# Kernel tuning notes

Hardware: AMD Instinct MI355X
Metric: run time of the kernel (lower is better)

Reference implementation:

```python
import jax, jax.numpy as jnp
import numpy as np

NX, NY, NT = 128, 128, 64          # global space-time grid
LX, LY = 2.0, 2.0                  # periodic domain extents
K_NB = 128                         # neighbors per query
NHEAD = 4
EPS = 1e-5


def setup_inputs() -> dict:
    key = jax.random.key(0)
    ks = jax.random.split(key, 12)
    N = NX * NY * NT
    B, d, dff, L = 2048, 64, 128, 2
    nrm = lambda k, s: jax.random.normal(k, s, jnp.float32) * 0.05
    return {
        "q_lin_idx": jax.random.randint(ks[0], (B,), 0, N),
        "offsets_ijk": jax.random.randint(ks[1], (K_NB, 3), 0, 8),
        "coords": jax.random.uniform(ks[2], (N, 3), jnp.float32) * 2.0,
        "vals": jax.random.normal(ks[3], (N, 3), jnp.float32),
        "log_gammas": jnp.zeros((3,), jnp.float32),
        "proj_w": nrm(ks[4], (d, 6)), "proj_b": jnp.zeros((d,), jnp.float32),
        "qkv_w": nrm(ks[5], (L, 3 * d, d)), "qkv_b": jnp.zeros((L, 3 * d), jnp.float32),
        "out_w": nrm(ks[6], (L, d, d)), "out_b": jnp.zeros((L, d), jnp.float32),
        "ln1_s": jnp.ones((L, d), jnp.float32), "ln1_b": jnp.zeros((L, d), jnp.float32),
        "ff1_w": nrm(ks[7], (L, dff, d)), "ff1_b": jnp.zeros((L, dff), jnp.float32),
        "ff2_w": nrm(ks[8], (L, d, dff)), "ff2_b": jnp.zeros((L, d), jnp.float32),
        "ln2_s": jnp.ones((L, d), jnp.float32), "ln2_b": jnp.zeros((L, d), jnp.float32),
        "head_ln_s": jnp.ones((d,), jnp.float32), "head_ln_b": jnp.zeros((d,), jnp.float32),
        "head1_w": nrm(ks[9], (d, d)), "head1_b": jnp.zeros((d,), jnp.float32),
        "head2_w": nrm(ks[10], (3, d)), "head2_b": jnp.zeros((3,), jnp.float32),
    }


def _ln(x, s, b):
    m = x.mean(-1, keepdims=True)
    v = ((x - m) ** 2).mean(-1, keepdims=True)
    return (x - m) * jax.lax.rsqrt(v + EPS) * s + b


def _dper(a, b, L):
    # periodic relative delta in [-L/2, L/2)
    return (a - b + 0.5 * L) % L - 0.5 * L


def reference(q_lin_idx, offsets_ijk, coords, vals, log_gammas, proj_w, proj_b,
              qkv_w, qkv_b, out_w, out_b, ln1_s, ln1_b, ff1_w, ff1_b, ff2_w, ff2_b,
              ln2_s, ln2_b, head_ln_s, head_ln_b, head1_w, head1_b, head2_w, head2_b):
    # --- periodic-wrapped neighbor indices (div/mod on linear index) ---
    i = q_lin_idx // (NY * NT)
    r = q_lin_idx % (NY * NT)
    j = r // NT
    kk = r % NT
    di, dj, dk = offsets_ijk[:, 0], offsets_ijk[:, 1], offsets_ijk[:, 2]
    I = (i[:, None] + di[None, :]) % NX          # wrap_x
    J = (j[:, None] + dj[None, :]) % NY          # wrap_y
    T = jnp.clip(kk[:, None] + dk[None, :], 0, NT - 1)  # no wrap in t
    nb = I * (NY * NT) + J * NT + T              # [B, K]

    # --- gather + relative-delta encode ---
    q_xyz = coords[q_lin_idx]                    # [B, 3]
    nb_xyz = coords[nb]                          # [B, K, 3]
    dx = _dper(nb_xyz[..., 0], q_xyz[:, None, 0], LX)
    dy = _dper(nb_xyz[..., 1], q_xyz[:, None, 1], LY)
    dt = nb_xyz[..., 2] - q_xyz[:, None, 2]
    rel = jnp.stack([dx, dy, dt], -1) * jnp.exp(log_gammas)[None, None, :]
    tokens = jnp.concatenate([rel, vals[nb]], -1)  # [B, K, 6]

    # --- input projection + TransformerEncoder (post-norm, relu FF) ---
    h = tokens @ proj_w.T + proj_b               # [B, S, d]
    B, S, d = h.shape
    dh = d // NHEAD
    scale = 1.0 / np.sqrt(dh).astype(np.float32)
    for l in range(qkv_w.shape[0]):
        qkv = h @ qkv_w[l].T + qkv_b[l]
        qh, kh, vh = jnp.split(qkv, 3, axis=-1)
        qh = qh.reshape(B, S, NHEAD, dh).transpose(0, 2, 1, 3)
        kh = kh.reshape(B, S, NHEAD, dh).transpose(0, 2, 1, 3)
        vh = vh.reshape(B, S, NHEAD, dh).transpose(0, 2, 1, 3)
        att = jax.nn.softmax(jnp.einsum('bhqd,bhkd->bhqk', qh, kh) * scale, axis=-1)
        o = jnp.einsum('bhqk,bhkd->bhqd', att, vh).transpose(0, 2, 1, 3).reshape(B, S, d)
        h = _ln(h + (o @ out_w[l].T + out_b[l]), ln1_s[l], ln1_b[l])
        ff = jax.nn.relu(h @ ff1_w[l].T + ff1_b[l]) @ ff2_w[l].T + ff2_b[l]
        h = _ln(h + ff, ln2_s[l], ln2_b[l])

    # --- mean pool over neighbors + head ---
    hm = h.mean(axis=1)                          # [B, d]
    g = _ln(hm, head_ln_s, head_ln_b)
    g = jax.nn.gelu(g @ head1_w.T + head1_b, approximate=False)
    return g @ head2_w.T + head2_b               # [B, 3]
```

## Files before the change

### kernel.cpp

```cpp
#include <hip/hip_runtime.h>
#include <math.h>

#define NXg 128
#define NYg 128
#define NTg 64
#define SEQ 128
#define DIM 64
#define NH 4
#define DHd 16
#define DFFd 128
#define NLAYER 2
#define EPSf 1e-5f

typedef _Float16 f16x8 __attribute__((ext_vector_type(8)));
typedef _Float16 f16x4 __attribute__((ext_vector_type(4)));
typedef float f32x4 __attribute__((ext_vector_type(4)));

#define MFMA16(a, b, c) __builtin_amdgcn_mfma_f32_16x16x32_f16(a, b, c, 0, 0, 0)

__device__ __forceinline__ f16x8 zero8() {
  f16x8 z;
#pragma unroll
  for (int i = 0; i < 8; ++i) z[i] = (_Float16)0.0f;
  return z;
}
__device__ __forceinline__ f16x8 ld8(const _Float16* p) { return *(const f16x8*)p; }

__global__ void prep_weights(const float* __restrict__ qkv_w,
                             const float* __restrict__ out_w,
                             const float* __restrict__ ff1_w,
                             const float* __restrict__ ff2_w,
                             _Float16* __restrict__ wsH) {
  int i = blockIdx.x * 256 + threadIdx.x;
  if (i < 24576) wsH[i] = (_Float16)qkv_w[i];
  else if (i < 32768) wsH[i] = (_Float16)out_w[i - 24576];
  else if (i < 49152) wsH[i] = (_Float16)ff1_w[i - 32768];
  else if (i < 65536) wsH[i] = (_Float16)ff2_w[i - 49152];
}

__device__ __forceinline__ void res_ln_T(f32x4 acc[4][2],
                                         const float* __restrict__ bias,
                                         const float* __restrict__ lns,
                                         const float* __restrict__ lnb,
                                         _Float16* sX,
                                         int wv, int quad, int l15) {
  f32x4 bb[4], sv[4], bv[4];
#pragma unroll
  for (int mt = 0; mt < 4; ++mt) {
    bb[mt] = *(const f32x4*)(bias + mt * 16 + quad * 4);
    sv[mt] = *(const f32x4*)(lns + mt * 16 + quad * 4);
    bv[mt] = *(const f32x4*)(lnb + mt * 16 + quad * 4);
  }
#pragma unroll
  for (int qt = 0; qt < 2; ++qt) {
    const int q = (wv * 2 + qt) * 16 + l15;
    float v[4][4];
#pragma unroll
    for (int mt = 0; mt < 4; ++mt) {
      f16x4 rx = *(const f16x4*)(sX + q * 72 + mt * 16 + quad * 4);
#pragma unroll
      for (int jr = 0; jr < 4; ++jr)
        v[mt][jr] = acc[mt][qt][jr] + bb[mt][jr] + (float)rx[jr];
    }
    float s = 0.f;
#pragma unroll
    for (int mt = 0; mt < 4; ++mt)
#pragma unroll
      for (int jr = 0; jr < 4; ++jr) s += v[mt][jr];
    s += __shfl_xor(s, 16, 64);
    s += __shfl_xor(s, 32, 64);
    const float mu = s * (1.0f / 64.0f);
    float q2 = 0.f;
#pragma unroll
    for (int mt = 0; mt < 4; ++mt)
#pragma unroll
      for (int jr = 0; jr < 4; ++jr) { float d = v[mt][jr] - mu; q2 = fmaf(d, d, q2); }
    q2 += __shfl_xor(q2, 16, 64);
    q2 += __shfl_xor(q2, 32, 64);
    const float rstd = rsqrtf(q2 * (1.0f / 64.0f) + EPSf);
#pragma unroll
    for (int mt = 0; mt < 4; ++mt) {
      f16x4 o;
#pragma unroll
      for (int jr = 0; jr < 4; ++jr)
        o[jr] = (_Float16)fmaf((v[mt][jr] - mu) * rstd, sv[mt][jr], bv[mt][jr]);
      *(f16x4*)(sX + q * 72 + mt * 16 + quad * 4) = o;
    }
  }
}

__global__ __launch_bounds__(256, 2)
void fieldformer_mfma(const int* __restrict__ q_lin_idx,
                      const int* __restrict__ offsets_ijk,
                      const float* __restrict__ coords,
                      const float* __restrict__ vals,
                      const float* __restrict__ log_gammas,
                      const float* __restrict__ proj_w,
                      const float* __restrict__ proj_b,
                      const float* __restrict__ qkv_b,
                      const float* __restrict__ out_b,
                      const float* __restrict__ ln1_s,
                      const float* __restrict__ ln1_b,
                      const float* __restrict__ ff1_b,
                      const float* __restrict__ ff2_b,
                      const float* __restrict__ ln2_s,
                      const float* __restrict__ ln2_b,
                      const float* __restrict__ head_ln_s,
                      const float* __restrict__ head_ln_b,
                      const float* __restrict__ head1_w,
                      const float* __restrict__ head1_b,
                      const float* __restrict__ head2_w,
                      const float* __restrict__ head2_b,
                      const _Float16* __restrict__ wH,
                      float* __restrict__ out) {
  __shared__ __align__(16) _Float16 sX[128 * 72];
  __shared__ __align__(16) _Float16 sPH[128 * 136];
  __shared__ __align__(16) _Float16 sQ[128 * 24];
  __shared__ __align__(16) _Float16 sK[128 * 24];
  __shared__ __align__(16) _Float16 sV[16 * 136];

  _Float16* sO = sQ;

  const int tid = threadIdx.x;
  const int wv = tid >> 6;
  const int lane = tid & 63;
  const int quad = lane >> 4;
  const int l15 = lane & 15;
  const int b = blockIdx.x;

  {
    const int row = tid >> 1, hf = tid & 1;
    const int q = q_lin_idx[b];
    const int qi = q / (NYg * NTg);
    const int qrem = q - qi * (NYg * NTg);
    const int qj = qrem / NTg;
    const int qk = qrem - qj * NTg;
    const int di = offsets_ijk[row * 3 + 0];
    const int dj = offsets_ijk[row * 3 + 1];
    const int dk = offsets_ijk[row * 3 + 2];
    const int I = (qi + di) % NXg;
    const int J = (qj + dj) % NYg;
    int T = qk + dk; T = T < 0 ? 0 : (T > NTg - 1 ? NTg - 1 : T);
    const int nb = I * (NYg * NTg) + J * NTg + T;
    const float qx = coords[q * 3 + 0], qy = coords[q * 3 + 1], qz = coords[q * 3 + 2];
    const float nx_ = coords[nb * 3 + 0], ny_ = coords[nb * 3 + 1], nz_ = coords[nb * 3 + 2];
    float ax = nx_ - qx + 1.0f; ax -= 2.0f * floorf(ax * 0.5f); ax -= 1.0f;
    float ay = ny_ - qy + 1.0f; ay -= 2.0f * floorf(ay * 0.5f); ay -= 1.0f;
    const float at = nz_ - qz;
    float tok[6];
    tok[0] = ax * expf(log_gammas[0]);
    tok[1] = ay * expf(log_gammas[1]);
    tok[2] = at * expf(log_gammas[2]);
    tok[3] = vals[nb * 3 + 0];
    tok[4] = vals[nb * 3 + 1];
    tok[5] = vals[nb * 3 + 2];
#pragma unroll
    for (int ci = 0; ci < 32; ++ci) {
      const int c = hf * 32 + ci;
      const float* w = proj_w + c * 6;
      float a = proj_b[c];
      a = fmaf(tok[0], w[0], a); a = fmaf(tok[1], w[1], a);
      a = fmaf(tok[2], w[2], a); a = fmaf(tok[3], w[3], a);
      a = fmaf(tok[4], w[4], a); a = fmaf(tok[5], w[5], a);
      sX[row * 72 + c] = (_Float16)a;
    }
  }
  __syncthreads();

  for (int l = 0; l < NLAYER; ++l) {
    const _Float16* qkvH = wH + l * 192 * 64;
    const _Float16* woutH = wH + 24576 + l * 64 * 64;
    const _Float16* ff1H = wH + 32768 + l * 128 * 64;
    const _Float16* ff2H = wH + 49152 + l * 64 * 128;
    const float* bqkv = qkv_b + l * 192;

    f16x8 bx[2][2];
#pragma unroll
    for (int qt = 0; qt < 2; ++qt)
#pragma unroll
      for (int kt = 0; kt < 2; ++kt)
        bx[qt][kt] = ld8(sX + ((wv * 2 + qt) * 16 + l15) * 72 + kt * 32 + quad * 8);

    f32x4 y2[4][2];
#pragma unroll
    for (int mt = 0; mt < 4; ++mt)
#pragma unroll
      for (int qt = 0; qt < 2; ++qt) y2[mt][qt] = f32x4{0.f, 0.f, 0.f, 0.f};

    for (int h = 0; h < NH; ++h) {
      f32x4 dq[2] = {f32x4{0.f,0.f,0.f,0.f}, f32x4{0.f,0.f,0.f,0.f}};
      f32x4 dk[2] = {f32x4{0.f,0.f,0.f,0.f}, f32x4{0.f,0.f,0.f,0.f}};
      f32x4 dv[2] = {f32x4{0.f,0.f,0.f,0.f}, f32x4{0.f,0.f,0.f,0.f}};
#pragma unroll
      for (int kt = 0; kt < 2; ++kt) {
        f16x8 awq = ld8(qkvH + (h * 16 + l15) * 64 + kt * 32 + quad * 8);
        f16x8 awk = ld8(qkvH + (64 + h * 16 + l15) * 64 + kt * 32 + quad * 8);
        f16x8 awv = ld8(qkvH + (128 + h * 16 + l15) * 64 + kt * 32 + quad * 8);
#pragma unroll
        for (int qt = 0; qt < 2; ++qt) {
          dq[qt] = MFMA16(awq, bx[qt][kt], dq[qt]);
          dk[qt] = MFMA16(awk, bx[qt][kt], dk[qt]);
          dv[qt] = MFMA16(awv, bx[qt][kt], dv[qt]);
        }
      }
      {
        const f32x4 bq4 = *(const f32x4*)(bqkv + h * 16 + quad * 4);
        const f32x4 bk4 = *(const f32x4*)(bqkv + 64 + h * 16 + quad * 4);
        const f32x4 bv4 = *(const f32x4*)(bqkv + 128 + h * 16 + quad * 4);
#pragma unroll
        for (int qt = 0; qt < 2; ++qt) {
          const int q = (wv * 2 + qt) * 16 + l15;
          f16x4 pq, pk;
#pragma unroll
          for (int jr = 0; jr < 4; ++jr) {
            pq[jr] = (_Float16)((dq[qt][jr] + bq4[jr]) * 0.25f);
            pk[jr] = (_Float16)(dk[qt][jr] + bk4[jr]);
            sV[(quad * 4 + jr) * 136 + q] = (_Float16)(dv[qt][jr] + bv4[jr]);
          }
          *(f16x4*)(sQ + q * 24 + quad * 4) = pq;
          *(f16x4*)(sK + q * 24 + quad * 4) = pk;
        }
      }
      __syncthreads();

      f16x8 bq[2];
#pragma unroll
      for (int qt = 0; qt < 2; ++qt)
        bq[qt] = (quad < 2) ? ld8(sQ + ((wv * 2 + qt) * 16 + l15) * 24 + quad * 8)
                            : zero8();
      f32x4 sc[8][2];
#pragma unroll
      for (int mt = 0; mt < 8; ++mt)
#pragma unroll
        for (int qt = 0; qt < 2; ++qt) sc[mt][qt] = f32x4{0.f, 0.f, 0.f, 0.f};
#pragma unroll
      for (int mt = 0; mt < 8; ++mt) {
        f16x8 ak = (quad < 2) ? ld8(sK + (mt * 16 + l15) * 24 + quad * 8) : zero8();
#pragma unroll
        for (int qt = 0; qt < 2; ++qt) sc[mt][qt] = MFMA16(ak, bq[qt], sc[mt][qt]);
      }

#pragma unroll
      for (int qt = 0; qt < 2; ++qt) {
        const int q = (wv * 2 + qt) * 16 + l15;
        float m0 = sc[0][qt][0];
#pragma unroll
        for (int mt = 0; mt < 8; ++mt)
#pragma unroll
          for (int jr = 0; jr < 4; ++jr) m0 = fmaxf(m0, sc[mt][qt][jr]);
        m0 = fmaxf(m0, __shfl_xor(m0, 16, 64));
        m0 = fmaxf(m0, __shfl_xor(m0, 32, 64));
        float s0 = 0.f;
#pragma unroll
        for (int mt = 0; mt < 8; ++mt)
#pragma unroll
          for (int jr = 0; jr < 4; ++jr) {
            float e = __expf(sc[mt][qt][jr] - m0);
            sc[mt][qt][jr] = e;
            s0 += e;
          }
        s0 += __shfl_xor(s0, 16, 64);
        s0 += __shfl_xor(s0, 32, 64);
        const float inv = 1.0f / s0;
#pragma unroll
        for (int mt = 0; mt < 8; ++mt) {
          f16x4 pp;
#pragma unroll
          for (int jr = 0; jr < 4; ++jr) pp[jr] = (_Float16)(sc[mt][qt][jr] * inv);
          *(f16x4*)(sPH + q * 136 + mt * 16 + quad * 4) = pp;
        }
      }

      f32x4 ov[2] = {f32x4{0.f,0.f,0.f,0.f}, f32x4{0.f,0.f,0.f,0.f}};
#pragma unroll
      for (int kt = 0; kt < 4; ++kt) {
        f16x8 av = ld8(sV + l15 * 136 + kt * 32 + quad * 8);
#pragma unroll
        for (int qt = 0; qt < 2; ++qt) {
          f16x8 bp = ld8(sPH + ((wv * 2 + qt) * 16 + l15) * 136 + kt * 32 + quad * 8);
          ov[qt] = MFMA16(av, bp, ov[qt]);
        }
      }
      __syncthreads();

#pragma unroll
      for (int qt = 0; qt < 2; ++qt) {
        const int q = (wv * 2 + qt) * 16 + l15;
        f16x4 po;
#pragma unroll
        for (int jr = 0; jr < 4; ++jr) po[jr] = (_Float16)ov[qt][jr];
        *(f16x4*)(sO + q * 24 + quad * 4) = po;
      }

      f16x8 bo[2];
#pragma unroll
      for (int qt = 0; qt < 2; ++qt)
        bo[qt] = (quad < 2) ? ld8(sO + ((wv * 2 + qt) * 16 + l15) * 24 + quad * 8)
                            : zero8();
#pragma unroll
      for (int mt = 0; mt < 4; ++mt) {
        f16x8 aw = (quad < 2) ? ld8(woutH + (mt * 16 + l15) * 64 + h * 16 + quad * 8)
                              : zero8();
#pragma unroll
        for (int qt = 0; qt < 2; ++qt) y2[mt][qt] = MFMA16(aw, bo[qt], y2[mt][qt]);
      }
    }

    res_ln_T(y2, out_b + l * 64, ln1_s + l * 64, ln1_b + l * 64, sX, wv, quad, l15);

    f32x4 f[8][2];
#pragma unroll
    for (int mt = 0; mt < 8; ++mt)
#pragma unroll
      for (int qt = 0; qt < 2; ++qt) f[mt][qt] = f32x4{0.f, 0.f, 0.f, 0.f};
#pragma unroll
    for (int kt = 0; kt < 2; ++kt) {
      f16x8 bxn[2];
#pragma unroll
      for (int qt = 0; qt < 2; ++qt)
        bxn[qt] = ld8(sX + ((wv * 2 + qt) * 16 + l15) * 72 + kt * 32 + quad * 8);
#pragma unroll
      for (int mt = 0; mt < 8; ++mt) {
        f16x8 aw = ld8(ff1H + (mt * 16 + l15) * 64 + kt * 32 + quad * 8);
#pragma unroll
        for (int qt = 0; qt < 2; ++qt) f[mt][qt] = MFMA16(aw, bxn[qt], f[mt][qt]);
      }
    }
    {
      const float* b1 = ff1_b + l * 128;
#pragma unroll
      for (int mt = 0; mt < 8; ++mt) {
        const f32x4 bb = *(const f32x4*)(b1 + mt * 16 + quad * 4);
#pragma unroll
        for (int qt = 0; qt < 2; ++qt) {
          const int q = (wv * 2 + qt) * 16 + l15;
          f16x4 ph;
#pragma unroll
          for (int jr = 0; jr < 4; ++jr)
            ph[jr] = (_Float16)fmaxf(f[mt][qt][jr] + bb[jr], 0.f);
          *(f16x4*)(sPH + q * 136 + mt * 16 + quad * 4) = ph;
        }
      }
    }

    f32x4 g[4][2];
#pragma unroll
    for (int mt = 0; mt < 4; ++mt)
#pragma unroll
      for (int qt = 0; qt < 2; ++qt) g[mt][qt] = f32x4{0.f, 0.f, 0.f, 0.f};
#pragma unroll
    for (int kt = 0; kt < 4; ++kt) {
      f16x8 bh[2];
#pragma unroll
      for (int qt = 0; qt < 2; ++qt)
        bh[qt] = ld8(sPH + ((wv * 2 + qt) * 16 + l15) * 136 + kt * 32 + quad * 8);
#pragma unroll
      for (int mt = 0; mt < 4; ++mt) {
        f16x8 aw = ld8(ff2H + (mt * 16 + l15) * 128 + kt * 32 + quad * 8);
#pragma unroll
        for (int qt = 0; qt < 2; ++qt) g[mt][qt] = MFMA16(aw, bh[qt], g[mt][qt]);
      }
    }
    res_ln_T(g, ff2_b + l * 64, ln2_s + l * 64, ln2_b + l * 64, sX, wv, quad, l15);
  }

  __syncthreads();
  {
    float* pf = (float*)sPH;
    float* gsc = pf + 256;
    float* asc = pf + 320;
    const int col = tid & 63, rg = tid >> 6;
    float s = 0.f;
    for (int rr = rg * 32; rr < rg * 32 + 32; ++rr) s += (float)sX[rr * 72 + col];
    pf[rg * 64 + col] = s;
    __syncthreads();
    if (tid < 64) {
      const float hm = (pf[tid] + pf[64 + tid] + pf[128 + tid] + pf[192 + tid]) * (1.0f / 128.0f);
      float t = hm;
      t += __shfl_xor(t, 1, 64);  t += __shfl_xor(t, 2, 64);
      t += __shfl_xor(t, 4, 64);  t += __shfl_xor(t, 8, 64);
      t += __shfl_xor(t, 16, 64); t += __shfl_xor(t, 32, 64);
      const float mu = t * (1.0f / 64.0f);
      const float dv = hm - mu;
      float v2 = dv * dv;
      v2 += __shfl_xor(v2, 1, 64);  v2 += __shfl_xor(v2, 2, 64);
      v2 += __shfl_xor(v2, 4, 64);  v2 += __shfl_xor(v2, 8, 64);
      v2 += __shfl_xor(v2, 16, 64); v2 += __shfl_xor(v2, 32, 64);
      const float var = v2 * (1.0f / 64.0f);
      gsc[tid] = fmaf(dv * rsqrtf(var + EPSf), head_ln_s[tid], head_ln_b[tid]);
    }
    __syncthreads();
    if (tid < 64) {
      float z = head1_b[tid];
      for (int k = 0; k < 64; ++k) z = fmaf(gsc[k], head1_w[tid * 64 + k], z);
      asc[tid] = 0.5f * z * (1.0f + erff(z * 0.70710678118654752f));
    }
    __syncthreads();
    if (tid < 3) {
      float z = head2_b[tid];
      for (int k = 0; k < 64; ++k) z = fmaf(asc[k], head2_w[tid * 64 + k], z);
      out[b * 3 + tid] = z;
    }
  }
}

extern "C" void kernel_launch(void* const* d_in, const int* in_sizes, int n_in,
                              void* d_out, int out_size, void* d_ws, size_t ws_size,
                              hipStream_t stream) {
  (void)n_in; (void)ws_size; (void)out_size;
  const int B = in_sizes[0];
  _Float16* wsH = (_Float16*)d_ws;

  prep_weights<<<dim3(256), dim3(256), 0, stream>>>(
      (const float*)d_in[7],
      (const float*)d_in[9],
      (const float*)d_in[13],
      (const float*)d_in[15],
      wsH);

  fieldformer_mfma<<<dim3(B), dim3(256), 0, stream>>>(
      (const int*)d_in[0],
      (const int*)d_in[1],
      (const float*)d_in[2],
      (const float*)d_in[3],
      (const float*)d_in[4],
      (const float*)d_in[5],
      (const float*)d_in[6],
      (const float*)d_in[8],
      (const float*)d_in[10],
      (const float*)d_in[11],
      (const float*)d_in[12],
      (const float*)d_in[14],
      (const float*)d_in[16],
      (const float*)d_in[17],
      (const float*)d_in[18],
      (const float*)d_in[19],
      (const float*)d_in[20],
      (const float*)d_in[21],
      (const float*)d_in[22],
      (const float*)d_in[23],
      (const float*)d_in[24],
      wsH,
      (float*)d_out);
}
```

Before: 348.9 us.

## Keep residual stream in registers and build MFMA fragments via lane shuffles

The per-token residual activations now live in fp32 registers instead of an LDS buffer. MFMA B-fragments for X, Q and the attention output are assembled with packed-half conversions and cross-lane shuffles rather than LDS store/load round trips. This removes the sX and sQ shared buffers, restructures attention and the FFN per query tile, drops the softmax max-subtraction, does the final mean-pool with shuffles, and raises launch bounds to 3 blocks per CU. The aim is less LDS traffic and footprint and higher occupancy. The cost is more register pressure and shuffle work, and skipping the max subtraction risks exp overflow if attention scores grow large.

Result: slower. 383.1 us (+9.8%).

```diff
diff --git a/kernel.cpp b/kernel.cpp
--- a/kernel.cpp
+++ b/kernel.cpp
@@ -14,9 +14,19 @@
 
 typedef _Float16 f16x8 __attribute__((ext_vector_type(8)));
 typedef _Float16 f16x4 __attribute__((ext_vector_type(4)));
+typedef __fp16 fp16x2 __attribute__((ext_vector_type(2)));
 typedef float f32x4 __attribute__((ext_vector_type(4)));
 
 #define MFMA16(a, b, c) __builtin_amdgcn_mfma_f32_16x16x32_f16(a, b, c, 0, 0, 0)
+
+union FragU { int d[4]; f16x8 v; };
+union H4U  { int d[2]; f16x4 v; };
+
+__device__ __forceinline__ int pk2(float a, float b) {
+  union { fp16x2 h; int i; } u;
+  u.h = __builtin_amdgcn_cvt_pkrtz(a, b);
+  return u.i;
+}
 
 __device__ __forceinline__ f16x8 zero8() {
   f16x8 z;
@@ -25,6 +35,73 @@
   return z;
 }
 __device__ __forceinline__ f16x8 ld8(const _Float16* p) { return *(const f16x8*)p; }
+
+__device__ __forceinline__ f16x8 frag_k16(f32x4 d4, int quad, int l15) {
+  int p0 = pk2(d4[0], d4[1]);
+  int p1 = pk2(d4[2], d4[3]);
+  int slA = ((2 * quad) * 16 + l15) & 63;
+  int slB = ((2 * quad + 1) * 16 + l15) & 63;
+  FragU u;
+  u.d[0] = __shfl(p0, slA, 64);
+  u.d[1] = __shfl(p1, slA, 64);
+  u.d[2] = __shfl(p0, slB, 64);
+  u.d[3] = __shfl(p1, slB, 64);
+  if (quad >= 2) { u.d[0] = 0; u.d[1] = 0; u.d[2] = 0; u.d[3] = 0; }
+  return u.v;
+}
+
+__device__ __forceinline__ f16x8 frag_k64(const int pk[4][2], int kt, int quad, int l15) {
+  const int slA = (2 * (quad & 1)) * 16 + l15;
+  const int slB = (2 * (quad & 1) + 1) * 16 + l15;
+  const bool hi = quad >= 2;
+  int a0 = __shfl(pk[2 * kt][0], slA, 64), b0 = __shfl(pk[2 * kt + 1][0], slA, 64);
+  int a1 = __shfl(pk[2 * kt][1], slA, 64), b1 = __shfl(pk[2 * kt + 1][1], slA, 64);
+  int a2 = __shfl(pk[2 * kt][0], slB, 64), b2 = __shfl(pk[2 * kt + 1][0], slB, 64);
+  int a3 = __shfl(pk[2 * kt][1], slB, 64), b3 = __shfl(pk[2 * kt + 1][1], slB, 64);
+  FragU u;
+  u.d[0] = hi ? b0 : a0;
+  u.d[1] = hi ? b1 : a1;
+  u.d[2] = hi ? b2 : a2;
+  u.d[3] = hi ? b3 : a3;
+  return u.v;
+}
+
+__device__ __forceinline__ void res_ln_qt(const f32x4 acc[4], f32x4 Xq[4],
+                                          const float* __restrict__ bias,
+                                          const float* __restrict__ lns,
+                                          const float* __restrict__ lnb,
+                                          int quad) {
+  float v[4][4];
+  float s = 0.f;
+#pragma unroll
+  for (int mt = 0; mt < 4; ++mt) {
+    f32x4 bb = *(const f32x4*)(bias + mt * 16 + quad * 4);
+#pragma unroll
+    for (int jr = 0; jr < 4; ++jr) {
+      v[mt][jr] = acc[mt][jr] + bb[jr] + Xq[mt][jr];
+      s += v[mt][jr];
+    }
+  }
+  s += __shfl_xor(s, 16, 64);
+  s += __shfl_xor(s, 32, 64);
+  const float mu = s * (1.0f / 64.0f);
+  float q2 = 0.f;
+#pragma unroll
+  for (int mt = 0; mt < 4; ++mt)
+#pragma unroll
+    for (int jr = 0; jr < 4; ++jr) { float d = v[mt][jr] - mu; q2 = fmaf(d, d, q2); }
+  q2 += __shfl_xor(q2, 16, 64);
+  q2 += __shfl_xor(q2, 32, 64);
+  const float rstd = rsqrtf(q2 * (1.0f / 64.0f) + EPSf);
+#pragma unroll
+  for (int mt = 0; mt < 4; ++mt) {
+    f32x4 sv = *(const f32x4*)(lns + mt * 16 + quad * 4);
+    f32x4 bv = *(const f32x4*)(lnb + mt * 16 + quad * 4);
+#pragma unroll
+    for (int jr = 0; jr < 4; ++jr)
+      Xq[mt][jr] = fmaf((v[mt][jr] - mu) * rstd, sv[jr], bv[jr]);
+  }
+}
 
 __global__ void prep_weights(const float* __restrict__ qkv_w,
                              const float* __restrict__ out_w,
@@ -38,58 +115,7 @@
   else if (i < 65536) wsH[i] = (_Float16)ff2_w[i - 49152];
 }
 
-__device__ __forceinline__ void res_ln_T(f32x4 acc[4][2],
-                                         const float* __restrict__ bias,
-                                         const float* __restrict__ lns,
-                                         const float* __restrict__ lnb,
-                                         _Float16* sX,
-                                         int wv, int quad, int l15) {
-  f32x4 bb[4], sv[4], bv[4];
-#pragma unroll
-  for (int mt = 0; mt < 4; ++mt) {
-    bb[mt] = *(const f32x4*)(bias + mt * 16 + quad * 4);
-    sv[mt] = *(const f32x4*)(lns + mt * 16 + quad * 4);
-    bv[mt] = *(const f32x4*)(lnb + mt * 16 + quad * 4);
-  }
-#pragma unroll
-  for (int qt = 0; qt < 2; ++qt) {
-    const int q = (wv * 2 + qt) * 16 + l15;
-    float v[4][4];
-#pragma unroll
-    for (int mt = 0; mt < 4; ++mt) {
-      f16x4 rx = *(const f16x4*)(sX + q * 72 + mt * 16 + quad * 4);
-#pragma unroll
-      for (int jr = 0; jr < 4; ++jr)
-        v[mt][jr] = acc[mt][qt][jr] + bb[mt][jr] + (float)rx[jr];
-    }
-    float s = 0.f;
-#pragma unroll
-    for (int mt = 0; mt < 4; ++mt)
-#pragma unroll
-      for (int jr = 0; jr < 4; ++jr) s += v[mt][jr];
-    s += __shfl_xor(s, 16, 64);
-    s += __shfl_xor(s, 32, 64);
-    const float mu = s * (1.0f / 64.0f);
-    float q2 = 0.f;
-#pragma unroll
-    for (int mt = 0; mt < 4; ++mt)
-#pragma unroll
-      for (int jr = 0; jr < 4; ++jr) { float d = v[mt][jr] - mu; q2 = fmaf(d, d, q2); }
-    q2 += __shfl_xor(q2, 16, 64);
-    q2 += __shfl_xor(q2, 32, 64);
-    const float rstd = rsqrtf(q2 * (1.0f / 64.0f) + EPSf);
-#pragma unroll
-    for (int mt = 0; mt < 4; ++mt) {
-      f16x4 o;
-#pragma unroll
-      for (int jr = 0; jr < 4; ++jr)
-        o[jr] = (_Float16)fmaf((v[mt][jr] - mu) * rstd, sv[mt][jr], bv[mt][jr]);
-      *(f16x4*)(sX + q * 72 + mt * 16 + quad * 4) = o;
-    }
-  }
-}
-
-__global__ __launch_bounds__(256, 2)
+__global__ __launch_bounds__(256, 3)
 void fieldformer_mfma(const int* __restrict__ q_lin_idx,
                       const int* __restrict__ offsets_ijk,
                       const float* __restrict__ coords,
@@ -113,13 +139,9 @@
                       const float* __restrict__ head2_b,
                       const _Float16* __restrict__ wH,
                       float* __restrict__ out) {
-  __shared__ __align__(16) _Float16 sX[128 * 72];
   __shared__ __align__(16) _Float16 sPH[128 * 136];
-  __shared__ __align__(16) _Float16 sQ[128 * 24];
   __shared__ __align__(16) _Float16 sK[128 * 24];
   __shared__ __align__(16) _Float16 sV[16 * 136];
-
-  _Float16* sO = sQ;
 
   const int tid = threadIdx.x;
   const int wv = tid >> 6;
@@ -162,10 +184,21 @@
       a = fmaf(tok[0], w[0], a); a = fmaf(tok[1], w[1], a);
       a = fmaf(tok[2], w[2], a); a = fmaf(tok[3], w[3], a);
       a = fmaf(tok[4], w[4], a); a = fmaf(tok[5], w[5], a);
-      sX[row * 72 + c] = (_Float16)a;
+      sPH[row * 136 + c] = (_Float16)a;
     }
   }
   __syncthreads();
+
+  f32x4 X[2][4];
+#pragma unroll
+  for (int qt = 0; qt < 2; ++qt) {
+    const int q = (wv * 2 + qt) * 16 + l15;
+#pragma unroll
+    for (int mt = 0; mt < 4; ++mt) {
+      f16x4 t = *(const f16x4*)(sPH + q * 136 + mt * 16 + quad * 4);
+      X[qt][mt] = f32x4{(float)t[0], (float)t[1], (float)t[2], (float)t[3]};
+    }
+  }
 
   for (int l = 0; l < NLAYER; ++l) {
     const _Float16* qkvH = wH + l * 192 * 64;
@@ -174,18 +207,24 @@
     const _Float16* ff2H = wH + 49152 + l * 64 * 128;
     const float* bqkv = qkv_b + l * 192;
 
-    f16x8 bx[2][2];
+    f16x8 bxf[2][2];
+#pragma unroll
+    for (int qt = 0; qt < 2; ++qt) {
+      int pkx[4][2];
+#pragma unroll
+      for (int mt = 0; mt < 4; ++mt) {
+        pkx[mt][0] = pk2(X[qt][mt][0], X[qt][mt][1]);
+        pkx[mt][1] = pk2(X[qt][mt][2], X[qt][mt][3]);
+      }
+#pragma unroll
+      for (int kt = 0; kt < 2; ++kt) bxf[qt][kt] = frag_k64(pkx, kt, quad, l15);
+    }
+
+    f32x4 y2[2][4];
 #pragma unroll
     for (int qt = 0; qt < 2; ++qt)
 #pragma unroll
-      for (int kt = 0; kt < 2; ++kt)
-        bx[qt][kt] = ld8(sX + ((wv * 2 + qt) * 16 + l15) * 72 + kt * 32 + quad * 8);
-
-    f32x4 y2[4][2];
-#pragma unroll
-    for (int mt = 0; mt < 4; ++mt)
-#pragma unroll
-      for (int qt = 0; qt < 2; ++qt) y2[mt][qt] = f32x4{0.f, 0.f, 0.f, 0.f};
+      for (int mt = 0; mt < 4; ++mt) y2[qt][mt] = f32x4{0.f, 0.f, 0.f, 0.f};
 
     for (int h = 0; h < NH; ++h) {
       f32x4 dq[2] = {f32x4{0.f,0.f,0.f,0.f}, f32x4{0.f,0.f,0.f,0.f}};
@@ -198,11 +237,12 @@
         f16x8 awv = ld8(qkvH + (128 + h * 16 + l15) * 64 + kt * 32 + quad * 8);
 #pragma unroll
         for (int qt = 0; qt < 2; ++qt) {
-          dq[qt] = MFMA16(awq, bx[qt][kt], dq[qt]);
-          dk[qt] = MFMA16(awk, bx[qt][kt], dk[qt]);
-          dv[qt] = MFMA16(awv, bx[qt][kt], dv[qt]);
-        }
-      }
+          dq[qt] = MFMA16(awq, bxf[qt][kt], dq[qt]);
+          dk[qt] = MFMA16(awk, bxf[qt][kt], dk[qt]);
+          dv[qt] = MFMA16(awv, bxf[qt][kt], dv[qt]);
+        }
+      }
+      f16x8 bqf[2];
       {
         const f32x4 bq4 = *(const f32x4*)(bqkv + h * 16 + quad * 4);
         const f32x4 bk4 = *(const f32x4*)(bqkv + 64 + h * 16 + quad * 4);
@@ -210,53 +250,39 @@
 #pragma unroll
         for (int qt = 0; qt < 2; ++qt) {
           const int q = (wv * 2 + qt) * 16 + l15;
-          f16x4 pq, pk;
-#pragma unroll
-          for (int jr = 0; jr < 4; ++jr) {
-            pq[jr] = (_Float16)((dq[qt][jr] + bq4[jr]) * 0.25f);
-            pk[jr] = (_Float16)(dk[qt][jr] + bk4[jr]);
+          H4U k4;
+          k4.d[0] = pk2(dk[qt][0] + bk4[0], dk[qt][1] + bk4[1]);
+          k4.d[1] = pk2(dk[qt][2] + bk4[2], dk[qt][3] + bk4[3]);
+          *(f16x4*)(sK + q * 24 + quad * 4) = k4.v;
+#pragma unroll
+          for (int jr = 0; jr < 4; ++jr)
             sV[(quad * 4 + jr) * 136 + q] = (_Float16)(dv[qt][jr] + bv4[jr]);
-          }
-          *(f16x4*)(sQ + q * 24 + quad * 4) = pq;
-          *(f16x4*)(sK + q * 24 + quad * 4) = pk;
+          f32x4 qv;
+#pragma unroll
+          for (int jr = 0; jr < 4; ++jr) qv[jr] = (dq[qt][jr] + bq4[jr]) * 0.25f;
+          bqf[qt] = frag_k16(qv, quad, l15);
         }
       }
       __syncthreads();
-
-      f16x8 bq[2];
-#pragma unroll
-      for (int qt = 0; qt < 2; ++qt)
-        bq[qt] = (quad < 2) ? ld8(sQ + ((wv * 2 + qt) * 16 + l15) * 24 + quad * 8)
-                            : zero8();
-      f32x4 sc[8][2];
-#pragma unroll
-      for (int mt = 0; mt < 8; ++mt)
-#pragma unroll
-        for (int qt = 0; qt < 2; ++qt) sc[mt][qt] = f32x4{0.f, 0.f, 0.f, 0.f};
-#pragma unroll
-      for (int mt = 0; mt < 8; ++mt) {
-        f16x8 ak = (quad < 2) ? ld8(sK + (mt * 16 + l15) * 24 + quad * 8) : zero8();
-#pragma unroll
-        for (int qt = 0; qt < 2; ++qt) sc[mt][qt] = MFMA16(ak, bq[qt], sc[mt][qt]);
-      }
 
 #pragma unroll
       for (int qt = 0; qt < 2; ++qt) {
         const int q = (wv * 2 + qt) * 16 + l15;
-        float m0 = sc[0][qt][0];
+        f32x4 sc[8];
+#pragma unroll
+        for (int mt = 0; mt < 8; ++mt) sc[mt] = f32x4{0.f, 0.f, 0.f, 0.f};
+#pragma unroll
+        for (int mt = 0; mt < 8; ++mt) {
+          f16x8 ak = (quad < 2) ? ld8(sK + (mt * 16 + l15) * 24 + quad * 8) : zero8();
+          sc[mt] = MFMA16(ak, bqf[qt], sc[mt]);
+        }
+        float s0 = 0.f;
 #pragma unroll
         for (int mt = 0; mt < 8; ++mt)
 #pragma unroll
-          for (int jr = 0; jr < 4; ++jr) m0 = fmaxf(m0, sc[mt][qt][jr]);
-        m0 = fmaxf(m0, __shfl_xor(m0, 16, 64));
-        m0 = fmaxf(m0, __shfl_xor(m0, 32, 64));
-        float s0 = 0.f;
-#pragma unroll
-        for (int mt = 0; mt < 8; ++mt)
-#pragma unroll
           for (int jr = 0; jr < 4; ++jr) {
-            float e = __expf(sc[mt][qt][jr] - m0);
-            sc[mt][qt][jr] = e;
+            float e = __expf(sc[mt][jr]);
+            sc[mt][jr] = e;
             s0 += e;
           }
         s0 += __shfl_xor(s0, 16, 64);
@@ -264,115 +290,109 @@
         const float inv = 1.0f / s0;
 #pragma unroll
         for (int mt = 0; mt < 8; ++mt) {
-          f16x4 pp;
-#pragma unroll
-          for (int jr = 0; jr < 4; ++jr) pp[jr] = (_Float16)(sc[mt][qt][jr] * inv);
-          *(f16x4*)(sPH + q * 136 + mt * 16 + quad * 4) = pp;
-        }
-      }
-
-      f32x4 ov[2] = {f32x4{0.f,0.f,0.f,0.f}, f32x4{0.f,0.f,0.f,0.f}};
+          H4U pp;
+          pp.d[0] = pk2(sc[mt][0], sc[mt][1]);
+          pp.d[1] = pk2(sc[mt][2], sc[mt][3]);
+          *(f16x4*)(sPH + q * 136 + mt * 16 + quad * 4) = pp.v;
+        }
+        f32x4 ov = f32x4{0.f, 0.f, 0.f, 0.f};
+#pragma unroll
+        for (int kt = 0; kt < 4; ++kt) {
+          f16x8 av = ld8(sV + l15 * 136 + kt * 32 + quad * 8);
+          f16x8 bp = ld8(sPH + q * 136 + kt * 32 + quad * 8);
+          ov = MFMA16(av, bp, ov);
+        }
+#pragma unroll
+        for (int jr = 0; jr < 4; ++jr) ov[jr] *= inv;
+        f16x8 bof = frag_k16(ov, quad, l15);
+#pragma unroll
+        for (int mt = 0; mt < 4; ++mt) {
+          f16x8 aw = (quad < 2) ? ld8(woutH + (mt * 16 + l15) * 64 + h * 16 + quad * 8)
+                                : zero8();
+          y2[qt][mt] = MFMA16(aw, bof, y2[qt][mt]);
+        }
+      }
+      __syncthreads();
+    }
+
+#pragma unroll
+    for (int qt = 0; qt < 2; ++qt)
+      res_ln_qt(y2[qt], X[qt], out_b + l * 64, ln1_s + l * 64, ln1_b + l * 64, quad);
+
+#pragma unroll
+    for (int qt = 0; qt < 2; ++qt) {
+      int pkx[4][2];
+#pragma unroll
+      for (int mt = 0; mt < 4; ++mt) {
+        pkx[mt][0] = pk2(X[qt][mt][0], X[qt][mt][1]);
+        pkx[mt][1] = pk2(X[qt][mt][2], X[qt][mt][3]);
+      }
+#pragma unroll
+      for (int kt = 0; kt < 2; ++kt) bxf[qt][kt] = frag_k64(pkx, kt, quad, l15);
+    }
+
+#pragma unroll
+    for (int qt = 0; qt < 2; ++qt) {
+      const int q = (wv * 2 + qt) * 16 + l15;
+      f32x4 f8[8];
+#pragma unroll
+      for (int mt = 0; mt < 8; ++mt) f8[mt] = f32x4{0.f, 0.f, 0.f, 0.f};
+#pragma unroll
+      for (int kt = 0; kt < 2; ++kt)
+#pragma unroll
+        for (int mt = 0; mt < 8; ++mt) {
+          f16x8 aw = ld8(ff1H + (mt * 16 + l15) * 64 + kt * 32 + quad * 8);
+          f8[mt] = MFMA16(aw, bxf[qt][kt], f8[mt]);
+        }
+      const float* b1 = ff1_b + l * 128;
+#pragma unroll
+      for (int mt = 0; mt < 8; ++mt) {
+        f32x4 bb = *(const f32x4*)(b1 + mt * 16 + quad * 4);
+        H4U hh;
+        hh.d[0] = pk2(fmaxf(f8[mt][0] + bb[0], 0.f), fmaxf(f8[mt][1] + bb[1], 0.f));
+        hh.d[1] = pk2(fmaxf(f8[mt][2] + bb[2], 0.f), fmaxf(f8[mt][3] + bb[3], 0.f));
+        *(f16x4*)(sPH + q * 136 + mt * 16 + quad * 4) = hh.v;
+      }
+    }
+
+#pragma unroll
+    for (int qt = 0; qt < 2; ++qt) {
+      const int q = (wv * 2 + qt) * 16 + l15;
+      f32x4 g4[4];
+#pragma unroll
+      for (int mt = 0; mt < 4; ++mt) g4[mt] = f32x4{0.f, 0.f, 0.f, 0.f};
 #pragma unroll
       for (int kt = 0; kt < 4; ++kt) {
-        f16x8 av = ld8(sV + l15 * 136 + kt * 32 + quad * 8);
-#pragma unroll
-        for (int qt = 0; qt < 2; ++qt) {
-          f16x8 bp = ld8(sPH + ((wv * 2 + qt) * 16 + l15) * 136 + kt * 32 + quad * 8);
-          ov[qt] = MFMA16(av, bp, ov[qt]);
-        }
-      }
-      __syncthreads();
-
-#pragma unroll
-      for (int qt = 0; qt < 2; ++qt) {
-        const int q = (wv * 2 + qt) * 16 + l15;
-        f16x4 po;
-#pragma unroll
-        for (int jr = 0; jr < 4; ++jr) po[jr] = (_Float16)ov[qt][jr];
-        *(f16x4*)(sO + q * 24 + quad * 4) = po;
-      }
-
-      f16x8 bo[2];
-#pragma unroll
-      for (int qt = 0; qt < 2; ++qt)
-        bo[qt] = (quad < 2) ? ld8(sO + ((wv * 2 + qt) * 16 + l15) * 24 + quad * 8)
-                            : zero8();
-#pragma unroll
-      for (int mt = 0; mt < 4; ++mt) {
-        f16x8 aw = (quad < 2) ? ld8(woutH + (mt * 16 + l15) * 64 + h * 16 + quad * 8)
-                              : zero8();
-#pragma unroll
-        for (int qt = 0; qt < 2; ++qt) y2[mt][qt] = MFMA16(aw, bo[qt], y2[mt][qt]);
-      }
-    }
-
-    res_ln_T(y2, out_b + l * 64, ln1_s + l * 64, ln1_b + l * 64, sX, wv, quad, l15);
-
-    f32x4 f[8][2];
-#pragma unroll
-    for (int mt = 0; mt < 8; ++mt)
-#pragma unroll
-      for (int qt = 0; qt < 2; ++qt) f[mt][qt] = f32x4{0.f, 0.f, 0.f, 0.f};
-#pragma unroll
-    for (int kt = 0; kt < 2; ++kt) {
-      f16x8 bxn[2];
-#pragma unroll
-      for (int qt = 0; qt < 2; ++qt)
-        bxn[qt] = ld8(sX + ((wv * 2 + qt) * 16 + l15) * 72 + kt * 32 + quad * 8);
-#pragma unroll
-      for (int mt = 0; mt < 8; ++mt) {
-        f16x8 aw = ld8(ff1H + (mt * 16 + l15) * 64 + kt * 32 + quad * 8);
-#pragma unroll
-        for (int qt = 0; qt < 2; ++qt) f[mt][qt] = MFMA16(aw, bxn[qt], f[mt][qt]);
-      }
-    }
-    {
-      const float* b1 = ff1_b + l * 128;
-#pragma unroll
-      for (int mt = 0; mt < 8; ++mt) {
-        const f32x4 bb = *(const f32x4*)(b1 + mt * 16 + quad * 4);
-#pragma unroll
-        for (int qt = 0; qt < 2; ++qt) {
-          const int q = (wv * 2 + qt) * 16 + l15;
-          f16x4 ph;
-#pragma unroll
-          for (int jr = 0; jr < 4; ++jr)
-            ph[jr] = (_Float16)fmaxf(f[mt][qt][jr] + bb[jr], 0.f);
-          *(f16x4*)(sPH + q * 136 + mt * 16 + quad * 4) = ph;
-        }
-      }
-    }
-
-    f32x4 g[4][2];
-#pragma unroll
-    for (int mt = 0; mt < 4; ++mt)
-#pragma unroll
-      for (int qt = 0; qt < 2; ++qt) g[mt][qt] = f32x4{0.f, 0.f, 0.f, 0.f};
-#pragma unroll
-    for (int kt = 0; kt < 4; ++kt) {
-      f16x8 bh[2];
-#pragma unroll
-      for (int qt = 0; qt < 2; ++qt)
-        bh[qt] = ld8(sPH + ((wv * 2 + qt) * 16 + l15) * 136 + kt * 32 + quad * 8);
-#pragma unroll
-      for (int mt = 0; mt < 4; ++mt) {
-        f16x8 aw = ld8(ff2H + (mt * 16 + l15) * 128 + kt * 32 + quad * 8);
-#pragma unroll
-        for (int qt = 0; qt < 2; ++qt) g[mt][qt] = MFMA16(aw, bh[qt], g[mt][qt]);
-      }
-    }
-    res_ln_T(g, ff2_b + l * 64, ln2_s + l * 64, ln2_b + l * 64, sX, wv, quad, l15);
+        f16x8 bh = ld8(sPH + q * 136 + kt * 32 + quad * 8);
+#pragma unroll
+        for (int mt = 0; mt < 4; ++mt) {
+          f16x8 aw = ld8(ff2H + (mt * 16 + l15) * 128 + kt * 32 + quad * 8);
+          g4[mt] = MFMA16(aw, bh, g4[mt]);
+        }
+      }
+      res_ln_qt(g4, X[qt], ff2_b + l * 64, ln2_s + l * 64, ln2_b + l * 64, quad);
+    }
   }
 
   __syncthreads();
   {
-    float* pf = (float*)sPH;
+    float* pf = (float*)sK;
     float* gsc = pf + 256;
-    float* asc = pf + 320;
-    const int col = tid & 63, rg = tid >> 6;
-    float s = 0.f;
-    for (int rr = rg * 32; rr < rg * 32 + 32; ++rr) s += (float)sX[rr * 72 + col];
-    pf[rg * 64 + col] = s;
+    float* asc = gsc + 64;
+    f32x4 cs[4];
+#pragma unroll
+    for (int mt = 0; mt < 4; ++mt) cs[mt] = X[0][mt] + X[1][mt];
+#pragma unroll
+    for (int d = 1; d <= 8; d <<= 1)
+#pragma unroll
+      for (int mt = 0; mt < 4; ++mt)
+#pragma unroll
+        for (int jr = 0; jr < 4; ++jr) cs[mt][jr] += __shfl_xor(cs[mt][jr], d, 64);
+    if (l15 == 0) {
+#pragma unroll
+      for (int mt = 0; mt < 4; ++mt)
+        *(f32x4*)(pf + wv * 64 + mt * 16 + quad * 4) = cs[mt];
+    }
     __syncthreads();
     if (tid < 64) {
       const float hm = (pf[tid] + pf[64 + tid] + pf[128 + tid] + pf[192 + tid]) * (1.0f / 128.0f);
```
